# Optimization experiments

Hardware: AMD Instinct MI355X
Metric: run time of the kernel (lower is better)

The kernel has to match this reference:

```python
import jax, jax.numpy as jnp
import numpy as np

STRIDE = 16
MIN_SIZE = 16.0
NMS_THRESH = 0.7
N_PRE = 6000   # n_test_pre_nms
N_POST = 300   # n_test_post_nms
B, C_IN, FH, FW = 2, 256, 50, 50
A_PER = 9


def make_anchors(fh, fw):
    scales = np.array([8.0, 16.0, 32.0])
    ratios = np.array([0.5, 1.0, 2.0])
    ws, hs = [], []
    for r in ratios:
        for s in scales:
            size = s * STRIDE
            ws.append(size * np.sqrt(1.0 / r))
            hs.append(size * np.sqrt(r))
    wh = np.stack([np.array(ws), np.array(hs)], -1).reshape(1, 1, A_PER, 2)
    cx = (np.arange(fw) + 0.5) * STRIDE
    cy = (np.arange(fh) + 0.5) * STRIDE
    cyg, cxg = np.meshgrid(cy, cx, indexing='ij')
    ctr = np.stack([cxg, cyg], -1).reshape(fh, fw, 1, 2)
    anch = np.concatenate([ctr - wh / 2.0, ctr + wh / 2.0], -1)  # [fh,fw,9,4] xyxy
    return anch.reshape(-1, 4).astype(np.float32)


def conv2d(x, w, b, pad):
    y = jax.lax.conv_general_dilated(x, w, (1, 1), pad,
                                     dimension_numbers=('NCHW', 'OIHW', 'NCHW'))
    return y + b[None, :, None, None]


def decode_boxes(anchors, loc, img_w, img_h):
    # anchors [1,A,4] xyxy, loc [B,A,4] (dx,dy,dw,dh)
    aw = anchors[..., 2] - anchors[..., 0]
    ah = anchors[..., 3] - anchors[..., 1]
    acx = anchors[..., 0] + 0.5 * aw
    acy = anchors[..., 1] + 0.5 * ah
    cx = acx + loc[..., 0] * aw
    cy = acy + loc[..., 1] * ah
    w = aw * jnp.exp(loc[..., 2])
    h = ah * jnp.exp(loc[..., 3])
    x1 = jnp.clip(cx - 0.5 * w, 0.0, img_w)
    y1 = jnp.clip(cy - 0.5 * h, 0.0, img_h)
    x2 = jnp.clip(cx + 0.5 * w, 0.0, img_w)
    y2 = jnp.clip(cy + 0.5 * h, 0.0, img_h)
    return jnp.stack([x1, y1, x2, y2], -1)


def pairwise_iou(b):
    area = (b[:, 2] - b[:, 0]) * (b[:, 3] - b[:, 1])
    ix1 = jnp.maximum(b[:, None, 0], b[None, :, 0])
    iy1 = jnp.maximum(b[:, None, 1], b[None, :, 1])
    ix2 = jnp.minimum(b[:, None, 2], b[None, :, 2])
    iy2 = jnp.minimum(b[:, None, 3], b[None, :, 3])
    inter = jnp.clip(ix2 - ix1, 0.0) * jnp.clip(iy2 - iy1, 0.0)
    return inter / (area[:, None] + area[None, :] - inter)


def nms_select(boxes, scores):
    # boxes [N_PRE,4] already sorted by score descending
    iou = jax.lax.stop_gradient(pairwise_iou(boxes))
    idxs = jnp.arange(N_PRE)
    def body(i, keep):
        sup = (iou[i] > NMS_THRESH) & (idxs > i) & keep[i]
        return keep & ~sup
    keep = jax.lax.fori_loop(0, N_PRE, body, jnp.ones((N_PRE,), bool))
    keep = keep & (scores >= 0.0)          # drop invalid (score forced to -1)
    rank = jnp.cumsum(keep)
    sel = keep & (rank <= N_POST)
    order = jnp.argsort(jnp.where(sel, idxs, N_PRE))  # kept idxs first, score order
    top = order[:N_POST]
    m = jnp.arange(N_POST) < jnp.sum(sel)
    out_b = jnp.where(m[:, None], boxes[top], 0.0)
    out_s = jnp.where(m, scores[top], 0.0)
    return out_b, out_s, m


def proposal_pipeline(boxes, scores):
    # per-image: boxes [A,4], scores [A]
    valid = ((boxes[:, 2] - boxes[:, 0]) >= MIN_SIZE) & \
            ((boxes[:, 3] - boxes[:, 1]) >= MIN_SIZE)
    s = jnp.where(valid, scores, -1.0)
    top_s, top_i = jax.lax.top_k(s, N_PRE)
    return nms_select(boxes[top_i], top_s)


def setup_inputs() -> dict:
    k = jax.random.split(jax.random.key(0), 4)
    x = jax.random.normal(k[0], (B, C_IN, FH, FW), jnp.float32)
    conv1_w = 0.01 * jax.random.normal(k[1], (512, C_IN, 3, 3), jnp.float32)
    conv1_b = jnp.zeros((512,), jnp.float32)
    obj_w = 0.01 * jax.random.normal(k[2], (A_PER * 2, 512, 1, 1), jnp.float32)
    obj_b = jnp.zeros((A_PER * 2,), jnp.float32)
    loc_w = 0.01 * jax.random.normal(k[3], (A_PER * 4, 512, 1, 1), jnp.float32)
    loc_b = jnp.zeros((A_PER * 4,), jnp.float32)
    anchor_boxes = jnp.asarray(make_anchors(FH, FW))[None]  # [1, 22500, 4]
    return {"x": x, "conv1_w": conv1_w, "conv1_b": conv1_b,
            "obj_w": obj_w, "obj_b": obj_b, "loc_w": loc_w, "loc_b": loc_b,
            "anchor_boxes": anchor_boxes, "img_h": 800, "img_w": 800}


def reference(x, conv1_w, conv1_b, obj_w, obj_b, loc_w, loc_b, anchor_boxes, img_h, img_w):
    # RPN
    h = jax.nn.relu(conv2d(x, conv1_w, conv1_b, 'SAME'))
    loc = conv2d(h, loc_w, loc_b, 'VALID').transpose(0, 2, 3, 1).reshape(x.shape[0], -1, 4)
    obj = conv2d(h, obj_w, obj_b, 'VALID').transpose(0, 2, 3, 1).reshape(x.shape[0], -1, 2)
    # PreprocessHead: objectness prob, box decode, filter + sort + NMS
    scores = jax.nn.softmax(obj, axis=-1)[..., 1]                       # [B, A]
    boxes = decode_boxes(anchor_boxes[0][None], loc, float(img_w), float(img_h))  # [B, A, 4]
    out_boxes, out_scores, out_mask = jax.vmap(proposal_pipeline)(boxes, scores)
    return out_boxes, out_scores, out_mask
```

## Files before the change

kernel.cpp:

```cpp
#include <hip/hip_runtime.h>
#include <stdint.h>

#define NPOS 2500
#define NANCH 22500
#define NPRE 6000
#define NW 94
#define XPAD 2704
#define CMAX 32
#define KFAST 2048

__device__ __forceinline__ void gl_lds4(const float* g, float* l) {
  __builtin_amdgcn_global_load_lds((const __attribute__((address_space(1))) void*)g,
                                   (__attribute__((address_space(3))) void*)l, 4, 0, 0);
}
__device__ __forceinline__ void gl_lds16(const float* g, float* l) {
  __builtin_amdgcn_global_load_lds((const __attribute__((address_space(1))) void*)g,
                                   (__attribute__((address_space(3))) void*)l, 16, 0, 0);
}

__global__ __launch_bounds__(256) void prep(const float* __restrict__ w,
                                            float* __restrict__ wt,
                                            const float* __restrict__ x,
                                            float* __restrict__ xp,
                                            const float* __restrict__ objw,
                                            const float* __restrict__ locw,
                                            float* __restrict__ wt54b) {
  __shared__ float tile[32][33];
  int bid = blockIdx.x;
  int tid = threadIdx.x;
  if (bid < 1152) {
    int k0 = (bid % 72) * 32;
    int o0 = (bid / 72) * 32;
    int tx = tid & 31;
    int ty = tid >> 5;
#pragma unroll
    for (int i = 0; i < 4; ++i) {
      int oc = o0 + ty + i * 8;
      int kp = k0 + tx;
      tile[ty + i * 8][tx] = w[(size_t)oc * 2304 + kp];
    }
    __syncthreads();
#pragma unroll
    for (int i = 0; i < 4; ++i) {
      int kp = k0 + ty + i * 8;
      int ic = kp / 9, tap = kp % 9;
      wt[((size_t)tap * 256 + ic) * 512 + (o0 + tx)] = tile[tx][ty + i * 8];
    }
  } else if (bid < 6560) {
    int t = (bid - 1152) * 256 + tid;
    if (t < 2 * 256 * XPAD) {
      int c = t / XPAD;
      int r = t % XPAD;
      int yy = r / 52, xx = r % 52;
      float v = 0.f;
      if (yy >= 1 && yy <= 50 && xx >= 1 && xx <= 50)
        v = x[(size_t)c * NPOS + (yy - 1) * 50 + (xx - 1)];
      xp[t] = v;
    }
  } else {
    int t = (bid - 6560) * 256 + tid;
    if (t < 54 * 512) {
      int oc = t / 512, k = t % 512;
      float v = (oc < 18) ? objw[(size_t)oc * 512 + k] : locw[(size_t)(oc - 18) * 512 + k];
      wt54b[((size_t)(k >> 2) * 64 + oc) * 4 + (k & 3)] = v;
    }
  }
}

__global__ __launch_bounds__(256) void conv1_gemm(const float* __restrict__ xp,
                                                  const float* __restrict__ wt,
                                                  const float* __restrict__ bias,
                                                  float* __restrict__ h) {
  __shared__ __align__(16) float As[32][64];
  __shared__ __align__(16) float Bs[32][64];
  int b = blockIdx.z;
  int m0 = blockIdx.x * 64;
  int oc0 = blockIdx.y * 64;
  int tid = threadIdx.x;
  int lane = tid & 63;
  int wv = tid >> 6;
  int tn = tid & 15, tm = tid >> 4;
  float acc[4][4] = {};

  int p = m0 + lane;
  int pc = p < NPOS ? p : (NPOS - 1);
  int py = pc / 50, px = pc % 50;
  const float* gA0 = xp + (size_t)b * 256 * XPAD + py * 52 + px + 53;
  int brow = lane >> 4, bcol4 = (lane & 15) * 4;

  for (int tap = 0; tap < 9; ++tap) {
    int ky = tap / 3 - 1, kx = tap % 3 - 1;
    int koff = ky * 52 + kx;
    for (int icc = 0; icc < 8; ++icc) {
      int ic0 = icc * 32;
      __syncthreads();
#pragma unroll
      for (int j = 0; j < 8; ++j) {
        int kk = wv * 8 + j;
        gl_lds4(gA0 + (size_t)(ic0 + kk) * XPAD + koff, &As[kk][0]);
      }
#pragma unroll
      for (int q = 0; q < 2; ++q) {
        int r0 = wv * 8 + q * 4;
        gl_lds16(wt + ((size_t)tap * 256 + ic0 + r0 + brow) * 512 + oc0 + bcol4,
                 &Bs[r0][0]);
      }
      __syncthreads();
#pragma unroll
      for (int kk = 0; kk < 32; ++kk) {
        float4 av = *(const float4*)&As[kk][tm * 4];
        float4 bv = *(const float4*)&Bs[kk][tn * 4];
        float am[4] = {av.x, av.y, av.z, av.w};
        float bn[4] = {bv.x, bv.y, bv.z, bv.w};
#pragma unroll
        for (int i = 0; i < 4; ++i)
#pragma unroll
          for (int j = 0; j < 4; ++j) acc[i][j] = fmaf(am[i], bn[j], acc[i][j]);
      }
    }
  }
#pragma unroll
  for (int i = 0; i < 4; ++i) {
    int pp = m0 + tm * 4 + i;
    if (pp < NPOS) {
      float4 v;
      float* vp = (float*)&v;
#pragma unroll
      for (int j = 0; j < 4; ++j) {
        int oc = oc0 + tn * 4 + j;
        vp[j] = fmaxf(acc[i][j] + bias[oc], 0.f);
      }
      *(float4*)&h[((size_t)b * NPOS + pp) * 512 + oc0 + tn * 4] = v;
    }
  }
}

__global__ __launch_bounds__(64) void heads(const float* __restrict__ h,
                                            const float* __restrict__ wt54b,
                                            const float* __restrict__ objb,
                                            const float* __restrict__ locb,
                                            const float* __restrict__ anch,
                                            const int* __restrict__ imgh,
                                            const int* __restrict__ imgw,
                                            float* __restrict__ scores,
                                            float4* __restrict__ boxes) {
  __shared__ float hv[4 * 512];
  __shared__ float outs[4][64];
  int blk = blockIdx.x;
  int b = blk / 625;
  int p0 = (blk % 625) * 4;
  int lane = threadIdx.x;
  const float4* hp4 = (const float4*)(h + ((size_t)b * NPOS + p0) * 512);
  float4* hv4 = (float4*)hv;
#pragma unroll
  for (int q = 0; q < 8; ++q) hv4[lane + 64 * q] = hp4[lane + 64 * q];
  __syncthreads();
  if (lane < 54) {
    float bias0 = (lane < 18) ? objb[lane] : locb[lane - 18];
    float a0 = bias0, a1 = bias0, a2 = bias0, a3 = bias0;
    const float4* w4 = (const float4*)wt54b;
#pragma unroll 4
    for (int k = 0; k < 128; ++k) {
      float4 wv = w4[k * 64 + lane];
      float4 h0 = hv4[k], h1 = hv4[128 + k], h2 = hv4[256 + k], h3 = hv4[384 + k];
      a0 = fmaf(wv.x, h0.x, a0); a0 = fmaf(wv.y, h0.y, a0);
      a0 = fmaf(wv.z, h0.z, a0); a0 = fmaf(wv.w, h0.w, a0);
      a1 = fmaf(wv.x, h1.x, a1); a1 = fmaf(wv.y, h1.y, a1);
      a1 = fmaf(wv.z, h1.z, a1); a1 = fmaf(wv.w, h1.w, a1);
      a2 = fmaf(wv.x, h2.x, a2); a2 = fmaf(wv.y, h2.y, a2);
      a2 = fmaf(wv.z, h2.z, a2); a2 = fmaf(wv.w, h2.w, a2);
      a3 = fmaf(wv.x, h3.x, a3); a3 = fmaf(wv.y, h3.y, a3);
      a3 = fmaf(wv.z, h3.z, a3); a3 = fmaf(wv.w, h3.w, a3);
    }
    outs[0][lane] = a0; outs[1][lane] = a1; outs[2][lane] = a2; outs[3][lane] = a3;
  }
  __syncthreads();
  if (lane < 36) {
    int pi = lane / 9, a = lane % 9;
    int p = p0 + pi;
    float l0 = outs[pi][2 * a], l1 = outs[pi][2 * a + 1];
    float mx = fmaxf(l0, l1);
    float e0 = expf(l0 - mx);
    float e1 = expf(l1 - mx);
    float s = e1 / (e0 + e1);
    float d0 = outs[pi][18 + 4 * a + 0];
    float d1 = outs[pi][18 + 4 * a + 1];
    float d2 = outs[pi][18 + 4 * a + 2];
    float d3 = outs[pi][18 + 4 * a + 3];
    int ai = p * 9 + a;
    float4 A = ((const float4*)anch)[ai];
    float aw = A.z - A.x, ah = A.w - A.y;
    float acx = A.x + 0.5f * aw, acy = A.y + 0.5f * ah;
    float cx = acx + d0 * aw, cy = acy + d1 * ah;
    float w = aw * expf(d2), hh = ah * expf(d3);
    float W = (float)imgw[0], H = (float)imgh[0];
    float x1 = fminf(fmaxf(cx - 0.5f * w, 0.f), W);
    float y1 = fminf(fmaxf(cy - 0.5f * hh, 0.f), H);
    float x2 = fminf(fmaxf(cx + 0.5f * w, 0.f), W);
    float y2 = fminf(fmaxf(cy + 0.5f * hh, 0.f), H);
    bool valid = (x2 - x1 >= 16.f) && (y2 - y1 >= 16.f);
    scores[(size_t)b * NANCH + ai] = valid ? s : -1.f;
    boxes[(size_t)b * NANCH + ai] = make_float4(x1, y1, x2, y2);
  }
}

__device__ inline unsigned int mono_of(float f) {
  unsigned int u = __float_as_uint(f);
  return (u & 0x80000000u) ? ~u : (u | 0x80000000u);
}

__device__ __forceinline__ unsigned int suffix_strict(unsigned int v,
                                                      unsigned int* partw,
                                                      int tid, int lane, int wv) {
  unsigned int inc = v;
#pragma unroll
  for (int d = 1; d < 64; d <<= 1) {
    unsigned int u = __shfl_down(inc, d, 64);
    if (lane + d < 64) inc += u;
  }
  if (lane == 0) partw[wv] = inc;
  __syncthreads();
  if (tid < 16) {
    unsigned int tot = partw[tid];
    unsigned int inc2 = tot;
#pragma unroll
    for (int d = 1; d < 16; d <<= 1) {
      unsigned int u = __shfl_down(inc2, d, 64);
      if (tid + d < 16) inc2 += u;
    }
    partw[tid] = inc2 - tot;
  }
  __syncthreads();
  return partw[wv] + (inc - v);
}

template <int KSEL, int SLOTK, int TBLSZ, bool GATED>
__global__ __launch_bounds__(1024) void topk_sort_t(const float* __restrict__ scores,
                                                    const float4* __restrict__ boxes,
                                                    float* __restrict__ sscore,
                                                    float4* __restrict__ sbox,
                                                    const unsigned int* __restrict__ state) {
  int b = blockIdx.x;
  if (GATED && state[b * 192 + 189]) return;
  const float* sc = scores + (size_t)b * NANCH;
  __shared__ unsigned int hist[4096];
  __shared__ unsigned int part[1024];
  __shared__ unsigned short pidA[SLOTK * 64];
  __shared__ unsigned short pidB[SLOTK * 64];
  __shared__ unsigned short table[TBLSZ];
  __shared__ int res[8];
  int tid = threadIdx.x;
  int lane = tid & 63;
  int wv = tid >> 6;

  for (int i = tid; i < 4096; i += 1024) hist[i] = 0;
  __syncthreads();
  for (int i = tid; i < NANCH; i += 1024) atomicAdd(&hist[mono_of(sc[i]) >> 20], 1u);
  __syncthreads();
  {
    unsigned int h0 = hist[4 * tid], h1 = hist[4 * tid + 1];
    unsigned int h2 = hist[4 * tid + 2], h3 = hist[4 * tid + 3];
    unsigned int c = suffix_strict(h0 + h1 + h2 + h3, part, tid, lane, wv);
    const unsigned int need = KSEL;
    if (c < need && c + h3 >= need) { res[0] = 4 * tid + 3; res[1] = (int)c; }
    c += h3;
    if (c < need && c + h2 >= need) { res[0] = 4 * tid + 2; res[1] = (int)c; }
    c += h2;
    if (c < need && c + h1 >= need) { res[0] = 4 * tid + 1; res[1] = (int)c; }
    c += h1;
    if (c < need && c + h0 >= need) { res[0] = 4 * tid + 0; res[1] = (int)c; }
  }
  __syncthreads();
  int t1 = res[0], a1 = res[1];
  __syncthreads();

  for (int i = tid; i < 4096; i += 1024) hist[i] = 0;
  __syncthreads();
  for (int i = tid; i < NANCH; i += 1024) {
    unsigned int m = mono_of(sc[i]);
    if ((int)(m >> 20) == t1) atomicAdd(&hist[(m >> 8) & 0xFFF], 1u);
  }
  __syncthreads();
  {
    unsigned int h0 = hist[4 * tid], h1 = hist[4 * tid + 1];
    unsigned int h2 = hist[4 * tid + 2], h3 = hist[4 * tid + 3];
    unsigned int c = suffix_strict(h0 + h1 + h2 + h3, part, tid, lane, wv);
    const unsigned int need = (unsigned)(KSEL - a1);
    if (c < need && c + h3 >= need) { res[2] = 4 * tid + 3; res[3] = (int)c; }
    c += h3;
    if (c < need && c + h2 >= need) { res[2] = 4 * tid + 2; res[3] = (int)c; }
    c += h2;
    if (c < need && c + h1 >= need) { res[2] = 4 * tid + 1; res[3] = (int)c; }
    c += h1;
    if (c < need && c + h0 >= need) { res[2] = 4 * tid + 0; res[3] = (int)c; }
  }
  __syncthreads();
  int t2 = res[2], a2 = res[3];
  __syncthreads();

  for (int i = tid; i < 256; i += 1024) hist[i] = 0;
  __syncthreads();
  unsigned int top24 = ((unsigned int)t1 << 12) | (unsigned int)t2;
  for (int i = tid; i < NANCH; i += 1024) {
    unsigned int m = mono_of(sc[i]);
    if ((m >> 8) == top24) atomicAdd(&hist[m & 0xFF], 1u);
  }
  __syncthreads();
  {
    unsigned int hb = (tid < 256) ? hist[tid] : 0;
    unsigned int c = suffix_strict(hb, part, tid, lane, wv);
    if (tid < 256) {
      const unsigned int need = (unsigned)(KSEL - a1 - a2);
      if (c < need && c + hb >= need) {
        res[4] = tid;
        res[6] = (int)(need - c);
        res[7] = (hb == need - c) ? NANCH : -1;
      }
    }
  }
  __syncthreads();
  int t3 = res[4];
  unsigned int T = (top24 << 8) | (unsigned int)t3;
  int ties_needed = res[6];
  int idx_cut = res[7];
  __syncthreads();

  if (idx_cut < 0) {
    for (int i = tid; i < 704; i += 1024) hist[i] = 0;
    __syncthreads();
    for (int i = tid; i < NANCH; i += 1024)
      if (mono_of(sc[i]) == T) atomicAdd(&hist[i >> 5], 1u);
    __syncthreads();
    if (tid == 0) {
      int c = 0, cut = NANCH;
      for (int bin = 0; bin < 704; ++bin) {
        int hc = (int)hist[bin];
        if (c + hc >= ties_needed) {
          int c2 = c;
          for (int idx = bin * 32; idx < bin * 32 + 32; ++idx) {
            if (idx < NANCH && mono_of(sc[idx]) == T) {
              ++c2;
              if (c2 == ties_needed) { cut = idx; break; }
            }
          }
          break;
        }
        c += hc;
      }
      res[7] = cut;
    }
    __syncthreads();
    idx_cut = res[7];
    __syncthreads();
  }

  int base0 = tid * 22;
  unsigned int selm = 0;
  int cnt = 0;
  for (int k = 0; k < 22; ++k) {
    int i = base0 + k;
    if (i < NANCH) {
      unsigned int m = mono_of(sc[i]);
      if (m > T || (m == T && i <= idx_cut)) { selm |= 1u << k; ++cnt; }
    }
  }
  {
    int inc = cnt;
#pragma unroll
    for (int d = 1; d < 64; d <<= 1) {
      int u = __shfl_up(inc, d, 64);
      if (lane >= d) inc += u;
    }
    if (lane == 63) part[wv] = (unsigned int)inc;
    __syncthreads();
    if (tid < 16) {
      int v = (int)part[tid];
      int inc2 = v;
#pragma unroll
      for (int d = 1; d < 16; d <<= 1) {
        int u = __shfl_up(inc2, d, 16);
        if (tid >= d) inc2 += u;
      }
      part[tid] = (unsigned int)(inc2 - v);
    }
    __syncthreads();
    int pos = (int)part[wv] + (inc - cnt);
    for (int k = 0; k < 22; ++k)
      if ((selm >> k) & 1u) pidA[pos++] = (unsigned short)(base0 + k);
  }
  __syncthreads();

  unsigned short* src = pidA;
  unsigned short* dst = pidB;
  constexpr int KITER = (SLOTK + 15) / 16;
  constexpr int VPT = TBLSZ / 1024;
  for (int pass = 0; pass < 6; ++pass) {
    int shift = pass * 6;
    for (int i = tid; i < TBLSZ; i += 1024) table[i] = 0;
    __syncthreads();
    int dig[KITER], irk[KITER], pidr[KITER];
#pragma unroll
    for (int k = 0; k < KITER; ++k) {
      dig[k] = 0; irk[k] = 0; pidr[k] = 0;
      int s = wv + 16 * k;
      if (s < SLOTK) {
        int e = s * 64 + lane;
        bool act = e < KSEL;
        int pid = act ? (int)src[e] : 0;
        unsigned int key = act ? ~mono_of(sc[pid]) : 0u;
        int d = (int)((key >> shift) & 63u);
        uint64_t peers = __ballot(act);
#pragma unroll
        for (int bb = 0; bb < 6; ++bb) {
          uint64_t bl = __ballot(((d >> bb) & 1) != 0);
          peers &= ((d >> bb) & 1) ? bl : ~bl;
        }
        if (act) {
          dig[k] = d;
          pidr[k] = pid;
          irk[k] = (int)__popcll(peers & ((1ull << lane) - 1ull));
          int leader = __ffsll((long long)peers) - 1;
          if (lane == leader)
            table[d * SLOTK + s] = (unsigned short)__popcll(peers);
        }
      }
    }
    __syncthreads();
    {
      int tb = tid * VPT;
      int v[VPT];
      int lsum = 0;
#pragma unroll
      for (int q = 0; q < VPT; ++q) { v[q] = table[tb + q]; lsum += v[q]; }
      int inc = lsum;
#pragma unroll
      for (int d = 1; d < 64; d <<= 1) {
        int u = __shfl_up(inc, d, 64);
        if (lane >= d) inc += u;
      }
      if (lane == 63) part[wv] = (unsigned int)inc;
      __syncthreads();
      if (tid < 16) {
        int vv = (int)part[tid];
        int inc2 = vv;
#pragma unroll
        for (int d = 1; d < 16; d <<= 1) {
          int u = __shfl_up(inc2, d, 16);
          if (tid >= d) inc2 += u;
        }
        part[tid] = (unsigned int)(inc2 - vv);
      }
      __syncthreads();
      int run = (int)part[wv] + (inc - lsum);
#pragma unroll
      for (int q = 0; q < VPT; ++q) { table[tb + q] = (unsigned short)run; run += v[q]; }
    }
    __syncthreads();
#pragma unroll
    for (int k = 0; k < KITER; ++k) {
      int s = wv + 16 * k;
      if (s < SLOTK) {
        int e = s * 64 + lane;
        if (e < KSEL) {
          int pos = (int)table[dig[k] * SLOTK + s] + irk[k];
          dst[pos] = (unsigned short)pidr[k];
        }
      }
    }
    __syncthreads();
    unsigned short* tmp = src; src = dst; dst = tmp;
  }

  for (int r = tid; r < KSEL; r += 1024) {
    int idx = (int)src[r];
    sscore[(size_t)b * NPRE + r] = sc[idx];
    sbox[(size_t)b * NPRE + r] = boxes[(size_t)b * NANCH + idx];
  }
}

__device__ __forceinline__ void iou_tile(const float4* __restrict__ sbox,
                                         uint64_t* __restrict__ M,
                                         int b, int it, int jt, int tid,
                                         float4* bi, float4* bj) {
  if (tid < 64) {
    int i = it * 64 + tid;
    bi[tid] = (i < NPRE) ? sbox[(size_t)b * NPRE + i] : make_float4(0, 0, 0, 0);
  }
  {
    int j = jt * 256 + tid;
    bj[tid] = (j < NPRE) ? sbox[(size_t)b * NPRE + j] : make_float4(0, 0, 0, 0);
  }
  __syncthreads();
  int li = tid & 63, wq = tid >> 6;
  int i = it * 64 + li;
  int w = jt * 4 + wq;
  if (i < NPRE && w < NW) {
    float4 A = bi[li];
    float areaA = (A.z - A.x) * (A.w - A.y);
    uint64_t bits = 0;
#pragma unroll 8
    for (int jj = 0; jj < 64; ++jj) {
      int j = w * 64 + jj;
      float4 Bx = bj[wq * 64 + jj];
      float ix1 = fmaxf(A.x, Bx.x), iy1 = fmaxf(A.y, Bx.y);
      float ix2 = fminf(A.z, Bx.z), iy2 = fminf(A.w, Bx.w);
      float inter = fmaxf(ix2 - ix1, 0.f) * fmaxf(iy2 - iy1, 0.f);
      float areaB = (Bx.z - Bx.x) * (Bx.w - Bx.y);
      float iou = inter / (areaA + areaB - inter);
      if ((j > i) && (j < NPRE) && (iou > 0.7f)) bits |= (1ull << jj);
    }
    M[((size_t)b * NPRE + i) * NW + w] = bits;
  }
}

__global__ __launch_bounds__(256) void iou_mat(const float4* __restrict__ sbox,
                                               uint64_t* __restrict__ M) {
  __shared__ float4 bi[64];
  __shared__ float4 bj[256];
  iou_tile(sbox, M, blockIdx.z, blockIdx.x, blockIdx.y, threadIdx.x, bi, bj);
}

__global__ __launch_bounds__(256) void iou_rest(const float4* __restrict__ sbox,
                                                uint64_t* __restrict__ M,
                                                const unsigned int* __restrict__ state) {
  if (state[blockIdx.z * 192 + 189]) return;
  int it = blockIdx.x, jt = blockIdx.y;
  if (it < CMAX && jt < CMAX / 4) return;
  __shared__ float4 bi[64];
  __shared__ float4 bj[256];
  iou_tile(sbox, M, blockIdx.z, it, jt, threadIdx.x, bi, bj);
}

__device__ inline uint64_t shfl64(uint64_t v, int src) {
  int lo = __shfl((int)(unsigned int)(v & 0xFFFFFFFFull), src, 64);
  int hi = __shfl((int)(unsigned int)(v >> 32), src, 64);
  return ((uint64_t)(unsigned int)hi << 32) | (unsigned int)lo;
}

__device__ __forceinline__ void nms_chunk(const uint64_t* __restrict__ Mb,
                                          const float* __restrict__ sscore,
                                          uint64_t* __restrict__ keep,
                                          int b, int c, int tid, int wlimit,
                                          unsigned int* supLo, unsigned int* supHi,
                                          int* klist, int* knS, int* countS) {
  int ibase = c * 64;
  if (tid < 64) {
    int lane = tid;
    if (lane == 0) *knS = 0;
    uint64_t supc = ((uint64_t)supHi[c] << 32) | supLo[c];
    uint64_t validm = (c == NW - 1) ? ((1ull << (NPRE - (NW - 1) * 64)) - 1ull) : ~0ull;
    int pos = ibase + lane;
    uint64_t myrow = (pos < NPRE) ? Mb[(size_t)pos * NW + c] : 0ull;
    bool sval = (pos < NPRE) && (sscore[(size_t)b * NPRE + pos] >= 0.f);
    uint64_t vb = __ballot(sval);
    uint64_t cur = validm & ~supc;
    uint64_t kept = 0;
    while (cur) {
      int i = __ffsll((long long)cur) - 1;
      kept |= (1ull << i);
      cur &= ~(1ull << i);
      uint64_t row = shfl64(myrow, i);
      cur &= ~row;
    }
    if (kept & (1ull << lane)) {
      int pp = atomicAdd(knS, 1);
      klist[pp] = lane;
    }
    if (lane == 0) {
      keep[b * NW + c] = kept;
      *countS += __popcll(kept & vb);
    }
  }
  __syncthreads();
  int kn = *knS;
  for (int t = tid; t < kn * 128; t += 1024) {
    int ii = t >> 7, w = t & 127;
    if (w > c && w < wlimit) {
      uint64_t row = Mb[(size_t)(ibase + klist[ii]) * NW + w];
      unsigned int lo = (unsigned int)row;
      unsigned int hi = (unsigned int)(row >> 32);
      if (lo) atomicOr(&supLo[w], lo);
      if (hi) atomicOr(&supHi[w], hi);
    }
  }
  __syncthreads();
}

__global__ __launch_bounds__(1024) void nms_scan(const uint64_t* __restrict__ M,
                                                 const float* __restrict__ sscore,
                                                 uint64_t* __restrict__ keep,
                                                 unsigned int* __restrict__ state) {
  __shared__ unsigned int supLo[NW], supHi[NW];
  __shared__ int klist[64];
  __shared__ int knS;
  __shared__ int countS;
  int b = blockIdx.x;
  int tid = threadIdx.x;
  const uint64_t* Mb = M + (size_t)b * NPRE * NW;

  for (int w = tid; w < NW; w += 1024) {
    supLo[w] = 0;
    supHi[w] = 0;
    keep[b * NW + w] = 0;
  }
  if (tid == 0) countS = 0;
  __syncthreads();

  int done = 0;
  for (int c = 0; c < CMAX; ++c) {
    nms_chunk(Mb, sscore, keep, b, c, tid, CMAX, supLo, supHi, klist, &knS, &countS);
    if (countS >= 300) { done = 1; break; }
  }
  __syncthreads();
  unsigned int* st = state + b * 192;
  for (int w = tid; w < NW; w += 1024) { st[w] = supLo[w]; st[94 + w] = supHi[w]; }
  if (tid == 0) { st[188] = (unsigned int)countS; st[189] = (unsigned int)done; }
}

__global__ __launch_bounds__(1024) void nms_finish(const uint64_t* __restrict__ M,
                                                   const float* __restrict__ sscore,
                                                   uint64_t* __restrict__ keep,
                                                   const unsigned int* __restrict__ state,
                                                   const float4* __restrict__ sbox,
                                                   float* __restrict__ out) {
  __shared__ unsigned int supLo[NW], supHi[NW];
  __shared__ int klist[64];
  __shared__ int knS;
  __shared__ int countS;
  __shared__ int cnt[128];
  __shared__ uint64_t fw[NW];
  int b = blockIdx.x;
  int tid = threadIdx.x;
  const uint64_t* Mb = M + (size_t)b * NPRE * NW;
  const unsigned int* st = state + b * 192;

  if (!st[189]) {
    for (int w = tid; w < NW; w += 1024) { supLo[w] = st[w]; supHi[w] = st[94 + w]; }
    if (tid == 0) countS = (int)st[188];
    __syncthreads();
    for (int c = 0; c < CMAX; ++c) {
      uint64_t kw = keep[b * NW + c];
      if (!kw) continue;
      int ibase = c * 64;
      const int WREST = NW - CMAX;
      for (int t = tid; t < 64 * WREST; t += 1024) {
        int j = t / WREST;
        int w = CMAX + (t % WREST);
        if ((kw >> j) & 1ull) {
          uint64_t row = Mb[(size_t)(ibase + j) * NW + w];
          unsigned int lo = (unsigned int)row;
          unsigned int hi = (unsigned int)(row >> 32);
          if (lo) atomicOr(&supLo[w], lo);
          if (hi) atomicOr(&supHi[w], hi);
        }
      }
    }
    __syncthreads();
    for (int c = CMAX; c < NW; ++c) {
      nms_chunk(Mb, sscore, keep, b, c, tid, NW, supLo, supHi, klist, &knS, &countS);
      if (countS >= 300) break;
    }
    __threadfence();
    __syncthreads();
  }

  for (int i = tid; i < 1200; i += 1024) out[b * 1200 + i] = 0.f;
  for (int i = tid; i < 300; i += 1024) {
    out[2400 + b * 300 + i] = 0.f;
    out[3000 + b * 300 + i] = 0.f;
  }
  uint64_t w = 0;
  if (tid < NW) {
    uint64_t kw = keep[b * NW + tid];
    while (kw) {
      int j = __ffsll((long long)kw) - 1;
      kw &= kw - 1;
      if (sscore[(size_t)b * NPRE + tid * 64 + j] >= 0.f) w |= (1ull << j);
    }
    fw[tid] = w;
  }
  if (tid < 128) cnt[tid] = (tid < NW) ? __popcll(w) : 0;
  __syncthreads();
  for (int off = 1; off < 128; off <<= 1) {
    int v = 0, u = 0;
    if (tid < 128) {
      v = cnt[tid];
      u = (tid >= off) ? cnt[tid - off] : 0;
    }
    __syncthreads();
    if (tid < 128) cnt[tid] = v + u;
    __syncthreads();
  }
  if (tid < NW) {
    int base = cnt[tid] - __popcll(fw[tid]);
    uint64_t ww = fw[tid];
    while (ww) {
      int j = __ffsll((long long)ww) - 1;
      ww &= ww - 1;
      if (base < 300) {
        int p = tid * 64 + j;
        float4 bx = sbox[(size_t)b * NPRE + p];
        float* ob = out + b * 1200 + base * 4;
        ob[0] = bx.x; ob[1] = bx.y; ob[2] = bx.z; ob[3] = bx.w;
        out[2400 + b * 300 + base] = sscore[(size_t)b * NPRE + p];
        out[3000 + b * 300 + base] = 1.0f;
      }
      ++base;
    }
  }
}

extern "C" void kernel_launch(void* const* d_in, const int* in_sizes, int n_in,
                              void* d_out, int out_size, void* d_ws, size_t ws_size,
                              hipStream_t stream) {
  const float* x       = (const float*)d_in[0];
  const float* conv1_w = (const float*)d_in[1];
  const float* conv1_b = (const float*)d_in[2];
  const float* obj_w   = (const float*)d_in[3];
  const float* obj_b   = (const float*)d_in[4];
  const float* loc_w   = (const float*)d_in[5];
  const float* loc_b   = (const float*)d_in[6];
  const float* anch    = (const float*)d_in[7];
  const int*   img_h   = (const int*)d_in[8];
  const int*   img_w   = (const int*)d_in[9];

  char* base = (char*)d_ws;
  float*        wt     = (float*)(base + 0);
  float*        h      = (float*)(base + 4718592);
  uint64_t*     M      = (uint64_t*)(base + 4718592);
  float*        scores = (float*)(base + 14958592);
  float4*       boxes  = (float4*)(base + 15138592);
  float*        sscore = (float*)(base + 15858592);
  float4*       sbox   = (float4*)(base + 15906592);
  uint64_t*     keep   = (uint64_t*)(base + 16098592);
  float*        xp     = (float*)(base + 16100096);
  unsigned int* state  = (unsigned int*)(base + 21637888);
  float*        wt54b  = (float*)(base + 15906592);

  hipLaunchKernelGGL(prep, dim3(6668), dim3(256), 0, stream,
                     conv1_w, wt, x, xp, obj_w, loc_w, wt54b);
  hipLaunchKernelGGL(conv1_gemm, dim3(40, 8, 2), dim3(256), 0, stream, xp, wt, conv1_b, h);
  hipLaunchKernelGGL(heads, dim3(1250), dim3(64), 0, stream, h, wt54b, obj_b, loc_b,
                     anch, img_h, img_w, scores, boxes);
  hipLaunchKernelGGL((topk_sort_t<KFAST, 32, 2048, false>), dim3(2), dim3(1024), 0, stream,
                     scores, boxes, sscore, sbox, state);
  hipLaunchKernelGGL(iou_mat, dim3(CMAX, CMAX / 4, 2), dim3(256), 0, stream, sbox, M);
  hipLaunchKernelGGL(nms_scan, dim3(2), dim3(1024), 0, stream, M, sscore, keep, state);
  hipLaunchKernelGGL((topk_sort_t<NPRE, 94, 6144, true>), dim3(2), dim3(1024), 0, stream,
                     scores, boxes, sscore, sbox, state);
  hipLaunchKernelGGL(iou_rest, dim3(NW, 24, 2), dim3(256), 0, stream, sbox, M, state);
  hipLaunchKernelGGL(nms_finish, dim3(2), dim3(1024), 0, stream, M, sscore, keep, state,
                     sbox, (float*)d_out);
}
```

Baseline: 403.6 us.

## Double-buffer conv1 GEMM with single-wave blocks and 8x8 register tiles

Restructures the 3x3 conv GEMM to run one 64-thread wave per block, with each thread computing an 8x8 output tile. LDS staging is now double-buffered and uses vmcnt waits instead of block barriers, so global-to-LDS loads for the next K chunk overlap compute on the current one. The aim is to raise FMA-to-LDS-read ratio and hide load latency. In exchange, the grid stays at 640 blocks of a single wave each, which lowers occupancy and per-CU parallelism. It also reorders two FMAs in the heads kernel.

```diff
diff --git a/kernel.cpp b/kernel.cpp
--- a/kernel.cpp
+++ b/kernel.cpp
@@ -67,20 +67,21 @@
   }
 }
 
-__global__ __launch_bounds__(256) void conv1_gemm(const float* __restrict__ xp,
-                                                  const float* __restrict__ wt,
-                                                  const float* __restrict__ bias,
-                                                  float* __restrict__ h) {
-  __shared__ __align__(16) float As[32][64];
-  __shared__ __align__(16) float Bs[32][64];
+__global__ __launch_bounds__(64) void conv1_gemm(const float* __restrict__ xp,
+                                                 const float* __restrict__ wt,
+                                                 const float* __restrict__ bias,
+                                                 float* __restrict__ h) {
+  __shared__ __align__(16) float As0[32][64];
+  __shared__ __align__(16) float Bs0[32][64];
+  __shared__ __align__(16) float As1[32][64];
+  __shared__ __align__(16) float Bs1[32][64];
   int b = blockIdx.z;
   int m0 = blockIdx.x * 64;
   int oc0 = blockIdx.y * 64;
-  int tid = threadIdx.x;
-  int lane = tid & 63;
-  int wv = tid >> 6;
-  int tn = tid & 15, tm = tid >> 4;
-  float acc[4][4] = {};
+  int lane = threadIdx.x;
+  int tm8 = (lane >> 3) * 8;
+  int tn8 = (lane & 7) * 8;
+  float acc[8][8] = {};
 
   int p = m0 + lane;
   int pc = p < NPOS ? p : (NPOS - 1);
@@ -88,49 +89,62 @@
   const float* gA0 = xp + (size_t)b * 256 * XPAD + py * 52 + px + 53;
   int brow = lane >> 4, bcol4 = (lane & 15) * 4;
 
-  for (int tap = 0; tap < 9; ++tap) {
-    int ky = tap / 3 - 1, kx = tap % 3 - 1;
-    int koff = ky * 52 + kx;
-    for (int icc = 0; icc < 8; ++icc) {
-      int ic0 = icc * 32;
-      __syncthreads();
-#pragma unroll
-      for (int j = 0; j < 8; ++j) {
-        int kk = wv * 8 + j;
-        gl_lds4(gA0 + (size_t)(ic0 + kk) * XPAD + koff, &As[kk][0]);
-      }
-#pragma unroll
-      for (int q = 0; q < 2; ++q) {
-        int r0 = wv * 8 + q * 4;
-        gl_lds16(wt + ((size_t)tap * 256 + ic0 + r0 + brow) * 512 + oc0 + bcol4,
-                 &Bs[r0][0]);
-      }
-      __syncthreads();
-#pragma unroll
-      for (int kk = 0; kk < 32; ++kk) {
-        float4 av = *(const float4*)&As[kk][tm * 4];
-        float4 bv = *(const float4*)&Bs[kk][tn * 4];
-        float am[4] = {av.x, av.y, av.z, av.w};
-        float bn[4] = {bv.x, bv.y, bv.z, bv.w};
-#pragma unroll
-        for (int i = 0; i < 4; ++i)
-#pragma unroll
-          for (int j = 0; j < 4; ++j) acc[i][j] = fmaf(am[i], bn[j], acc[i][j]);
-      }
-    }
-  }
-#pragma unroll
-  for (int i = 0; i < 4; ++i) {
-    int pp = m0 + tm * 4 + i;
+  auto stage = [&](int c, float (*Ad)[64], float (*Bd)[64]) {
+    int tap = c >> 3, icc = c & 7;
+    int koff = (tap / 3 - 1) * 52 + (tap % 3 - 1);
+    int ic0 = icc << 5;
+    const float* asrc = gA0 + (size_t)ic0 * XPAD + koff;
+#pragma unroll
+    for (int kk = 0; kk < 32; ++kk) gl_lds4(asrc + (size_t)kk * XPAD, &Ad[kk][0]);
+    const float* bsrc = wt + ((size_t)tap * 256 + ic0 + brow) * 512 + oc0 + bcol4;
+#pragma unroll
+    for (int q = 0; q < 8; ++q) gl_lds16(bsrc + (size_t)(q << 2) * 512, &Bd[q << 2][0]);
+  };
+
+  stage(0, As0, Bs0);
+  for (int c = 0; c < 72; ++c) {
+    float(*Ac)[64] = (c & 1) ? As1 : As0;
+    float(*Bc)[64] = (c & 1) ? Bs1 : Bs0;
+    if (c < 71) {
+      float(*An)[64] = (c & 1) ? As0 : As1;
+      float(*Bn)[64] = (c & 1) ? Bs0 : Bs1;
+      stage(c + 1, An, Bn);
+      asm volatile("s_waitcnt vmcnt(40)" ::: "memory");
+    } else {
+      asm volatile("s_waitcnt vmcnt(0)" ::: "memory");
+    }
+#pragma unroll 8
+    for (int kk = 0; kk < 32; ++kk) {
+      float4 a0 = *(const float4*)&Ac[kk][tm8];
+      float4 a1 = *(const float4*)&Ac[kk][tm8 + 4];
+      float4 b0 = *(const float4*)&Bc[kk][tn8];
+      float4 b1 = *(const float4*)&Bc[kk][tn8 + 4];
+      float am[8] = {a0.x, a0.y, a0.z, a0.w, a1.x, a1.y, a1.z, a1.w};
+      float bn[8] = {b0.x, b0.y, b0.z, b0.w, b1.x, b1.y, b1.z, b1.w};
+#pragma unroll
+      for (int i = 0; i < 8; ++i)
+#pragma unroll
+        for (int j = 0; j < 8; ++j) acc[i][j] = fmaf(am[i], bn[j], acc[i][j]);
+    }
+  }
+
+  float4 bs0 = *(const float4*)&bias[oc0 + tn8];
+  float4 bs1 = *(const float4*)&bias[oc0 + tn8 + 4];
+  float bb[8] = {bs0.x, bs0.y, bs0.z, bs0.w, bs1.x, bs1.y, bs1.z, bs1.w};
+#pragma unroll
+  for (int i = 0; i < 8; ++i) {
+    int pp = m0 + tm8 + i;
     if (pp < NPOS) {
-      float4 v;
-      float* vp = (float*)&v;
-#pragma unroll
-      for (int j = 0; j < 4; ++j) {
-        int oc = oc0 + tn * 4 + j;
-        vp[j] = fmaxf(acc[i][j] + bias[oc], 0.f);
-      }
-      *(float4*)&h[((size_t)b * NPOS + pp) * 512 + oc0 + tn * 4] = v;
+      float4 v0, v1;
+      float* vp0 = (float*)&v0;
+      float* vp1 = (float*)&v1;
+#pragma unroll
+      for (int j = 0; j < 4; ++j) vp0[j] = fmaxf(acc[i][j] + bb[j], 0.f);
+#pragma unroll
+      for (int j = 0; j < 4; ++j) vp1[j] = fmaxf(acc[i][4 + j] + bb[4 + j], 0.f);
+      float* hrow = &h[((size_t)b * NPOS + pp) * 512 + oc0 + tn8];
+      *(float4*)hrow = v0;
+      *(float4*)(hrow + 4) = v1;
     }
   }
 }
@@ -170,7 +184,7 @@
       a2 = fmaf(wv.x, h2.x, a2); a2 = fmaf(wv.y, h2.y, a2);
       a2 = fmaf(wv.z, h2.z, a2); a2 = fmaf(wv.w, h2.w, a2);
       a3 = fmaf(wv.x, h3.x, a3); a3 = fmaf(wv.y, h3.y, a3);
-      a3 = fmaf(wv.z, h3.z, a3); a3 = fmaf(wv.w, h3.w, a3);
+      a3 = fmaf(wv.w, h3.w, a3); a3 = fmaf(wv.z, h3.z, a3);
     }
     outs[0][lane] = a0; outs[1][lane] = a1; outs[2][lane] = a2; outs[3][lane] = a3;
   }
@@ -739,7 +753,7 @@
 
   hipLaunchKernelGGL(prep, dim3(6668), dim3(256), 0, stream,
                      conv1_w, wt, x, xp, obj_w, loc_w, wt54b);
-  hipLaunchKernelGGL(conv1_gemm, dim3(40, 8, 2), dim3(256), 0, stream, xp, wt, conv1_b, h);
+  hipLaunchKernelGGL(conv1_gemm, dim3(40, 8, 2), dim3(64), 0, stream, xp, wt, conv1_b, h);
   hipLaunchKernelGGL(heads, dim3(1250), dim3(64), 0, stream, h, wt54b, obj_b, loc_b,
                      anch, img_h, img_w, scores, boxes);
   hipLaunchKernelGGL((topk_sort_t<KFAST, 32, 2048, false>), dim3(2), dim3(1024), 0, stream,
```

After: 593.9 us. 1.47x slower.

## Use 128x128 conv tiles with split-K atomics and move bias+ReLU into heads

Applied to the files above, without the earlier changes.

Each conv1 GEMM block now computes a 128x128 output tile with an 8x8 register micro-tile per thread, and the 256 input channels are split four ways across blocks. Partial sums are combined into a zeroed h buffer with atomicAdd, so prep gains an extra zero-fill section for h. Bias and ReLU move out of the GEMM epilogue into the heads kernel's load of h. The aim is higher arithmetic intensity per LDS load while keeping enough blocks in flight, at the cost of atomic traffic, the zero-fill pass and more register pressure.

```diff
diff --git a/kernel.cpp b/kernel.cpp
--- a/kernel.cpp
+++ b/kernel.cpp
@@ -24,7 +24,8 @@
                                             float* __restrict__ xp,
                                             const float* __restrict__ objw,
                                             const float* __restrict__ locw,
-                                            float* __restrict__ wt54b) {
+                                            float* __restrict__ wt54b,
+                                            float* __restrict__ hz) {
   __shared__ float tile[32][33];
   int bid = blockIdx.x;
   int tid = threadIdx.x;
@@ -57,85 +58,96 @@
         v = x[(size_t)c * NPOS + (yy - 1) * 50 + (xx - 1)];
       xp[t] = v;
     }
-  } else {
+  } else if (bid < 6668) {
     int t = (bid - 6560) * 256 + tid;
     if (t < 54 * 512) {
       int oc = t / 512, k = t % 512;
       float v = (oc < 18) ? objw[(size_t)oc * 512 + k] : locw[(size_t)(oc - 18) * 512 + k];
       wt54b[((size_t)(k >> 2) * 64 + oc) * 4 + (k & 3)] = v;
     }
+  } else {
+    int t = (bid - 6668) * 256 + tid;
+    if (t < 640000) ((float4*)hz)[t] = make_float4(0.f, 0.f, 0.f, 0.f);
   }
 }
 
 __global__ __launch_bounds__(256) void conv1_gemm(const float* __restrict__ xp,
                                                   const float* __restrict__ wt,
-                                                  const float* __restrict__ bias,
                                                   float* __restrict__ h) {
-  __shared__ __align__(16) float As[32][64];
-  __shared__ __align__(16) float Bs[32][64];
+  __shared__ __align__(16) float As[32][128];
+  __shared__ __align__(16) float Bs[32][128];
   int b = blockIdx.z;
-  int m0 = blockIdx.x * 64;
-  int oc0 = blockIdx.y * 64;
+  int m0 = blockIdx.x * 128;
+  int oc0 = (blockIdx.y & 3) * 128;
+  int kh = blockIdx.y >> 2;
   int tid = threadIdx.x;
   int lane = tid & 63;
   int wv = tid >> 6;
-  int tn = tid & 15, tm = tid >> 4;
-  float acc[4][4] = {};
-
-  int p = m0 + lane;
-  int pc = p < NPOS ? p : (NPOS - 1);
-  int py = pc / 50, px = pc % 50;
-  const float* gA0 = xp + (size_t)b * 256 * XPAD + py * 52 + px + 53;
-  int brow = lane >> 4, bcol4 = (lane & 15) * 4;
+  int tm = tid >> 4;
+  int tn = tid & 15;
+  float acc[8][8] = {};
+
+  int p0r = m0 + lane;
+  int p0c = p0r < NPOS ? p0r : (NPOS - 1);
+  int p1r = m0 + 64 + lane;
+  int p1c = p1r < NPOS ? p1r : (NPOS - 1);
+  const float* gA0 = xp + (size_t)b * 256 * XPAD + (p0c / 50) * 52 + (p0c % 50) + 53;
+  const float* gA1 = xp + (size_t)b * 256 * XPAD + (p1c / 50) * 52 + (p1c % 50) + 53;
+  int brow = lane >> 5, bcol4 = (lane & 31) * 4;
 
   for (int tap = 0; tap < 9; ++tap) {
     int ky = tap / 3 - 1, kx = tap % 3 - 1;
     int koff = ky * 52 + kx;
-    for (int icc = 0; icc < 8; ++icc) {
-      int ic0 = icc * 32;
+#pragma unroll
+    for (int ii = 0; ii < 2; ++ii) {
+      int ic0 = (kh * 2 + ii) * 32;
       __syncthreads();
 #pragma unroll
       for (int j = 0; j < 8; ++j) {
         int kk = wv * 8 + j;
-        gl_lds4(gA0 + (size_t)(ic0 + kk) * XPAD + koff, &As[kk][0]);
-      }
-#pragma unroll
-      for (int q = 0; q < 2; ++q) {
-        int r0 = wv * 8 + q * 4;
+        const float* s = gA0 + (size_t)(ic0 + kk) * XPAD + koff;
+        gl_lds4(s, &As[kk][0]);
+        const float* s1 = gA1 + (size_t)(ic0 + kk) * XPAD + koff;
+        gl_lds4(s1, &As[kk][64]);
+      }
+#pragma unroll
+      for (int q = 0; q < 4; ++q) {
+        int r0 = wv * 8 + q * 2;
         gl_lds16(wt + ((size_t)tap * 256 + ic0 + r0 + brow) * 512 + oc0 + bcol4,
                  &Bs[r0][0]);
       }
       __syncthreads();
-#pragma unroll
+#pragma unroll 4
       for (int kk = 0; kk < 32; ++kk) {
-        float4 av = *(const float4*)&As[kk][tm * 4];
-        float4 bv = *(const float4*)&Bs[kk][tn * 4];
-        float am[4] = {av.x, av.y, av.z, av.w};
-        float bn[4] = {bv.x, bv.y, bv.z, bv.w};
-#pragma unroll
-        for (int i = 0; i < 4; ++i)
-#pragma unroll
-          for (int j = 0; j < 4; ++j) acc[i][j] = fmaf(am[i], bn[j], acc[i][j]);
-      }
-    }
-  }
-#pragma unroll
-  for (int i = 0; i < 4; ++i) {
-    int pp = m0 + tm * 4 + i;
-    if (pp < NPOS) {
-      float4 v;
-      float* vp = (float*)&v;
-#pragma unroll
-      for (int j = 0; j < 4; ++j) {
-        int oc = oc0 + tn * 4 + j;
-        vp[j] = fmaxf(acc[i][j] + bias[oc], 0.f);
-      }
-      *(float4*)&h[((size_t)b * NPOS + pp) * 512 + oc0 + tn * 4] = v;
+        float4 a0 = *(const float4*)&As[kk][tm * 4];
+        float4 a1 = *(const float4*)&As[kk][64 + tm * 4];
+        float4 b0 = *(const float4*)&Bs[kk][tn * 4];
+        float4 b1 = *(const float4*)&Bs[kk][64 + tn * 4];
+        float am[8] = {a0.x, a0.y, a0.z, a0.w, a1.x, a1.y, a1.z, a1.w};
+        float bn[8] = {b0.x, b0.y, b0.z, b0.w, b1.x, b1.y, b1.z, b1.w};
+#pragma unroll
+        for (int i = 0; i < 8; ++i)
+#pragma unroll
+          for (int j = 0; j < 8; ++j) acc[i][j] = fmaf(am[i], bn[j], acc[i][j]);
+      }
+    }
+  }
+#pragma unroll
+  for (int i = 0; i < 8; ++i) {
+    int row = m0 + ((i & 4) ? 64 : 0) + tm * 4 + (i & 3);
+    if (row < NPOS) {
+      float* hrow = &h[((size_t)b * NPOS + row) * 512 + oc0];
+#pragma unroll
+      for (int j = 0; j < 8; ++j) {
+        int col = ((j & 4) ? 64 : 0) + tn * 4 + (j & 3);
+        atomicAdd(&hrow[col], acc[i][j]);
+      }
     }
   }
 }
 
 __global__ __launch_bounds__(64) void heads(const float* __restrict__ h,
+                                            const float* __restrict__ convb,
                                             const float* __restrict__ wt54b,
                                             const float* __restrict__ objb,
                                             const float* __restrict__ locb,
@@ -151,9 +163,20 @@
   int p0 = (blk % 625) * 4;
   int lane = threadIdx.x;
   const float4* hp4 = (const float4*)(h + ((size_t)b * NPOS + p0) * 512);
+  const float4* cb4 = (const float4*)convb;
   float4* hv4 = (float4*)hv;
 #pragma unroll
-  for (int q = 0; q < 8; ++q) hv4[lane + 64 * q] = hp4[lane + 64 * q];
+  for (int q = 0; q < 8; ++q) {
+    int f = lane + 64 * q;
+    float4 a = hp4[f];
+    float4 bb = cb4[f & 127];
+    float4 r;
+    r.x = fmaxf(a.x + bb.x, 0.f);
+    r.y = fmaxf(a.y + bb.y, 0.f);
+    r.z = fmaxf(a.z + bb.z, 0.f);
+    r.w = fmaxf(a.w + bb.w, 0.f);
+    hv4[f] = r;
+  }
   __syncthreads();
   if (lane < 54) {
     float bias0 = (lane < 18) ? objb[lane] : locb[lane - 18];
@@ -737,11 +760,11 @@
   unsigned int* state  = (unsigned int*)(base + 21637888);
   float*        wt54b  = (float*)(base + 15906592);
 
-  hipLaunchKernelGGL(prep, dim3(6668), dim3(256), 0, stream,
-                     conv1_w, wt, x, xp, obj_w, loc_w, wt54b);
-  hipLaunchKernelGGL(conv1_gemm, dim3(40, 8, 2), dim3(256), 0, stream, xp, wt, conv1_b, h);
-  hipLaunchKernelGGL(heads, dim3(1250), dim3(64), 0, stream, h, wt54b, obj_b, loc_b,
-                     anch, img_h, img_w, scores, boxes);
+  hipLaunchKernelGGL(prep, dim3(9168), dim3(256), 0, stream,
+                     conv1_w, wt, x, xp, obj_w, loc_w, wt54b, h);
+  hipLaunchKernelGGL(conv1_gemm, dim3(20, 16, 2), dim3(256), 0, stream, xp, wt, h);
+  hipLaunchKernelGGL(heads, dim3(1250), dim3(64), 0, stream, h, conv1_b, wt54b,
+                     obj_b, loc_b, anch, img_h, img_w, scores, boxes);
   hipLaunchKernelGGL((topk_sort_t<KFAST, 32, 2048, false>), dim3(2), dim3(1024), 0, stream,
                      scores, boxes, sscore, sbox, state);
   hipLaunchKernelGGL(iou_mat, dim3(CMAX, CMAX / 4, 2), dim3(256), 0, stream, sbox, M);
```

Measured after the change: 482.4 us. 1.2x slower.

## Split conv1 GEMM over input channels with 128x128 tiles, reduce in heads

Applied to the files above, without the earlier changes.

Adds a split-K variant of the 3x3 conv GEMM that uses 128x128 output tiles with an 8x8 register tile per thread. Each block handles one quarter of the input channels and writes a partial result to its own buffer. The heads kernel then sums the four partials, adds the conv bias and applies ReLU while loading into shared memory. This aims for more arithmetic per shared-memory load while keeping enough blocks (20x16x2) to fill the GPU. The cost is four times the intermediate storage and extra memory traffic in heads, and the path is only taken when the workspace is large enough.

```diff
diff --git a/kernel.cpp b/kernel.cpp
--- a/kernel.cpp
+++ b/kernel.cpp
@@ -8,6 +8,7 @@
 #define XPAD 2704
 #define CMAX 32
 #define KFAST 2048
+#define HPART 2560000
 
 __device__ __forceinline__ void gl_lds4(const float* g, float* l) {
   __builtin_amdgcn_global_load_lds((const __attribute__((address_space(1))) void*)g,
@@ -67,10 +68,83 @@
   }
 }
 
-__global__ __launch_bounds__(256) void conv1_gemm(const float* __restrict__ xp,
-                                                  const float* __restrict__ wt,
-                                                  const float* __restrict__ bias,
-                                                  float* __restrict__ h) {
+__global__ __launch_bounds__(256) void conv1_gemm_split(const float* __restrict__ xp,
+                                                        const float* __restrict__ wt,
+                                                        float* __restrict__ hpart) {
+  __shared__ __align__(16) float As[32][128];
+  __shared__ __align__(16) float Bs[32][128];
+  int b = blockIdx.z;
+  int m0 = blockIdx.x * 128;
+  int oc0 = (blockIdx.y & 3) * 128;
+  int kh = blockIdx.y >> 2;
+  int tid = threadIdx.x;
+  int lane = tid & 63;
+  int wv = tid >> 6;
+  int tm = tid >> 4;
+  int tn = tid & 15;
+  float acc[8][8] = {};
+
+  int p0r = m0 + lane;
+  int p0c = p0r < NPOS ? p0r : (NPOS - 1);
+  int p1r = m0 + 64 + lane;
+  int p1c = p1r < NPOS ? p1r : (NPOS - 1);
+  const float* gA0 = xp + (size_t)b * 256 * XPAD + (p0c / 50) * 52 + (p0c % 50) + 53;
+  const float* gA1 = xp + (size_t)b * 256 * XPAD + (p1c / 50) * 52 + (p1c % 50) + 53;
+  int brow = lane >> 5, bcol4 = (lane & 31) * 4;
+
+  for (int tap = 0; tap < 9; ++tap) {
+    int ky = tap / 3 - 1, kx = tap % 3 - 1;
+    int koff = ky * 52 + kx;
+#pragma unroll
+    for (int ii = 0; ii < 2; ++ii) {
+      int ic0 = (kh * 2 + ii) * 32;
+      __syncthreads();
+#pragma unroll
+      for (int j = 0; j < 8; ++j) {
+        int kk = wv * 8 + j;
+        gl_lds4(gA0 + (size_t)(ic0 + kk) * XPAD + koff, &As[kk][0]);
+        gl_lds4(gA1 + (size_t)(ic0 + kk) * XPAD + koff, &As[kk][64]);
+      }
+#pragma unroll
+      for (int q = 0; q < 4; ++q) {
+        int r0 = wv * 8 + q * 2;
+        gl_lds16(wt + ((size_t)tap * 256 + ic0 + r0 + brow) * 512 + oc0 + bcol4,
+                 &Bs[r0][0]);
+      }
+      __syncthreads();
+#pragma unroll 4
+      for (int kk = 0; kk < 32; ++kk) {
+        float4 a0 = *(const float4*)&As[kk][tm * 4];
+        float4 a1 = *(const float4*)&As[kk][64 + tm * 4];
+        float4 b0 = *(const float4*)&Bs[kk][tn * 4];
+        float4 b1 = *(const float4*)&Bs[kk][64 + tn * 4];
+        float am[8] = {a0.x, a0.y, a0.z, a0.w, a1.x, a1.y, a1.z, a1.w};
+        float bn[8] = {b0.x, b0.y, b0.z, b0.w, b1.x, b1.y, b1.z, b1.w};
+#pragma unroll
+        for (int i = 0; i < 8; ++i)
+#pragma unroll
+          for (int j = 0; j < 8; ++j) acc[i][j] = fmaf(am[i], bn[j], acc[i][j]);
+      }
+    }
+  }
+  float* hp = hpart + (size_t)kh * HPART;
+#pragma unroll
+  for (int i = 0; i < 8; ++i) {
+    int row = m0 + ((i & 4) ? 64 : 0) + tm * 4 + (i & 3);
+    if (row < NPOS) {
+      float* hrow = &hp[((size_t)b * NPOS + row) * 512 + oc0];
+      float4 v0 = make_float4(acc[i][0], acc[i][1], acc[i][2], acc[i][3]);
+      float4 v1 = make_float4(acc[i][4], acc[i][5], acc[i][6], acc[i][7]);
+      *(float4*)&hrow[tn * 4] = v0;
+      *(float4*)&hrow[64 + tn * 4] = v1;
+    }
+  }
+}
+
+__global__ __launch_bounds__(256) void conv1_gemm_mono(const float* __restrict__ xp,
+                                                       const float* __restrict__ wt,
+                                                       const float* __restrict__ bias,
+                                                       float* __restrict__ h) {
   __shared__ __align__(16) float As[32][64];
   __shared__ __align__(16) float Bs[32][64];
   int b = blockIdx.z;
@@ -135,25 +209,50 @@
   }
 }
 
-__global__ __launch_bounds__(64) void heads(const float* __restrict__ h,
-                                            const float* __restrict__ wt54b,
-                                            const float* __restrict__ objb,
-                                            const float* __restrict__ locb,
-                                            const float* __restrict__ anch,
-                                            const int* __restrict__ imgh,
-                                            const int* __restrict__ imgw,
-                                            float* __restrict__ scores,
-                                            float4* __restrict__ boxes) {
+template <bool SPLIT>
+__global__ __launch_bounds__(64) void heads_t(const float* __restrict__ h,
+                                              const float* __restrict__ convb,
+                                              const float* __restrict__ wt54b,
+                                              const float* __restrict__ objb,
+                                              const float* __restrict__ locb,
+                                              const float* __restrict__ anch,
+                                              const int* __restrict__ imgh,
+                                              const int* __restrict__ imgw,
+                                              float* __restrict__ scores,
+                                              float4* __restrict__ boxes) {
   __shared__ float hv[4 * 512];
   __shared__ float outs[4][64];
   int blk = blockIdx.x;
   int b = blk / 625;
   int p0 = (blk % 625) * 4;
   int lane = threadIdx.x;
-  const float4* hp4 = (const float4*)(h + ((size_t)b * NPOS + p0) * 512);
+  const float4* h4 = (const float4*)h;
+  size_t base = ((size_t)b * NPOS + p0) * 128;
   float4* hv4 = (float4*)hv;
-#pragma unroll
-  for (int q = 0; q < 8; ++q) hv4[lane + 64 * q] = hp4[lane + 64 * q];
+  if (SPLIT) {
+    const float4* cb4 = (const float4*)convb;
+#pragma unroll
+    for (int q = 0; q < 8; ++q) {
+      int f = lane + 64 * q;
+      float4 s0 = h4[base + f];
+      float4 s1 = h4[(HPART / 4) + base + f];
+      float4 s2 = h4[2 * (HPART / 4) + base + f];
+      float4 s3 = h4[3 * (HPART / 4) + base + f];
+      float4 bb = cb4[f & 127];
+      float4 r;
+      r.x = fmaxf(((s0.x + s1.x) + s2.x) + s3.x + bb.x, 0.f);
+      r.y = fmaxf(((s0.y + s1.y) + s2.y) + s3.y + bb.y, 0.f);
+      r.z = fmaxf(((s0.z + s1.z) + s2.z) + s3.z + bb.z, 0.f);
+      r.w = fmaxf(((s0.w + s1.w) + s2.w) + s3.w + bb.w, 0.f);
+      hv4[f] = r;
+    }
+  } else {
+#pragma unroll
+    for (int q = 0; q < 8; ++q) {
+      int f = lane + 64 * q;
+      hv4[f] = h4[base + f];
+    }
+  }
   __syncthreads();
   if (lane < 54) {
     float bias0 = (lane < 18) ? objb[lane] : locb[lane - 18];
@@ -725,23 +824,47 @@
   const int*   img_w   = (const int*)d_in[9];
 
   char* base = (char*)d_ws;
-  float*        wt     = (float*)(base + 0);
-  float*        h      = (float*)(base + 4718592);
-  uint64_t*     M      = (uint64_t*)(base + 4718592);
-  float*        scores = (float*)(base + 14958592);
-  float4*       boxes  = (float4*)(base + 15138592);
-  float*        sscore = (float*)(base + 15858592);
-  float4*       sbox   = (float4*)(base + 15906592);
-  uint64_t*     keep   = (uint64_t*)(base + 16098592);
-  float*        xp     = (float*)(base + 16100096);
-  unsigned int* state  = (unsigned int*)(base + 21637888);
-  float*        wt54b  = (float*)(base + 15906592);
+  const size_t NEED_SPLIT = 52359424;
+  bool use_split = (ws_size >= NEED_SPLIT);
+
+  float* wt = (float*)(base + 0);
+  float* h;
+  uint64_t* M;
+  float* scores;
+  float4* boxes;
+  float* sscore;
+  float4* sbox;
+  uint64_t* keep;
+  float* xp;
+  unsigned int* state;
+  float* wt54b;
+
+  size_t off = 4718592;
+  h = (float*)(base + off);
+  M = (uint64_t*)(base + off);
+  off += use_split ? 40960000 : 10240000;
+  scores = (float*)(base + off); off += 180000;
+  boxes  = (float4*)(base + off); off += 720000;
+  sscore = (float*)(base + off); off += 48000;
+  sbox   = (float4*)(base + off);
+  wt54b  = (float*)sbox;
+  off += 192000;
+  keep   = (uint64_t*)(base + off); off += 1504;
+  xp     = (float*)(base + off); off += 5537792;
+  state  = (unsigned int*)(base + off);
 
   hipLaunchKernelGGL(prep, dim3(6668), dim3(256), 0, stream,
                      conv1_w, wt, x, xp, obj_w, loc_w, wt54b);
-  hipLaunchKernelGGL(conv1_gemm, dim3(40, 8, 2), dim3(256), 0, stream, xp, wt, conv1_b, h);
-  hipLaunchKernelGGL(heads, dim3(1250), dim3(64), 0, stream, h, wt54b, obj_b, loc_b,
-                     anch, img_h, img_w, scores, boxes);
+  if (use_split) {
+    hipLaunchKernelGGL(conv1_gemm_split, dim3(20, 16, 2), dim3(256), 0, stream, xp, wt, h);
+    hipLaunchKernelGGL((heads_t<true>), dim3(1250), dim3(64), 0, stream, h, conv1_b, wt54b,
+                       obj_b, loc_b, anch, img_h, img_w, scores, boxes);
+  } else {
+    hipLaunchKernelGGL(conv1_gemm_mono, dim3(40, 8, 2), dim3(256), 0, stream, xp, wt,
+                       conv1_b, h);
+    hipLaunchKernelGGL((heads_t<false>), dim3(1250), dim3(64), 0, stream, h, conv1_b, wt54b,
+                       obj_b, loc_b, anch, img_h, img_w, scores, boxes);
+  }
   hipLaunchKernelGGL((topk_sort_t<KFAST, 32, 2048, false>), dim3(2), dim3(1024), 0, stream,
                      scores, boxes, sscore, sbox, state);
   hipLaunchKernelGGL(iou_mat, dim3(CMAX, CMAX / 4, 2), dim3(256), 0, stream, sbox, M);
```

After: 378.6 us. -6.2%, faster.
